# Kernel tuning notes

Measured on AMD Instinct MI355X. Metric: run time of the kernel, lower is better.

Reference implementation:

```python
import jax, jax.numpy as jnp
import numpy as np

R, A, B = 32, 16, 65536  # rules, antecedents, samples


def setup_inputs() -> dict:
    key = jax.random.key(0)
    k1, k2, k3 = jax.random.split(key, 3)
    input_data = jax.random.normal(k1, (B, A), dtype=jnp.float32)
    # abs(normal) like the original init; shift/scale keeps sigmas >= 1 so the
    # product of A Gaussian memberships stays well above fp32 underflow.
    FRB_W = jnp.abs(jax.random.normal(k2, (2 * R * A,), dtype=jnp.float32)) * 0.5 + 1.0
    C = jnp.abs(jax.random.normal(k3, (R, A + 1), dtype=jnp.float32))
    return {"input_data": input_data, "FRB_W": FRB_W, "C": C}


def reference(input_data, FRB_W, C):
    Rn = C.shape[0]
    An = C.shape[1] - 1
    # Faithful to the original indexing: locat_num = A*i + k, Gauss1 mf uses
    # FRB_weights[locat_num : locat_num+2] = (sigma, center) (overlapping windows).
    idx = jnp.arange(Rn)[:, None] * An + jnp.arange(An)[None, :]  # [R, A]
    sigma = FRB_W[idx]          # [R, A]
    center = FRB_W[idx + 1]     # [R, A]
    # Gauss1mf(x, [sigma, c]) = exp(-0.5 * ((x - c) / sigma)^2)
    z = (input_data[:, None, :] - center[None]) / sigma[None]      # [B, R, A]
    u = jnp.exp(-0.5 * z * z)                                      # [B, R, A]
    UU = jnp.prod(u, axis=-1)                                      # [B, R] rule firing strengths
    # TSK first-order consequent: C[:,0] bias + C[:,1:] @ x
    C_help = input_data @ C[:, 1:].T + C[:, 0]                     # [B, R]
    # weighted average over rules
    return jnp.sum(UU * C_help, axis=-1) / jnp.sum(UU, axis=-1)    # [B]
```

## Files before the change

kernel.cpp:

```cpp
#include <hip/hip_runtime.h>

#define RR 32
#define AA 16
#define SPLIT 4
#define RPW (RR / SPLIT)
#define BLOCK 256
#define SPB 64


__global__ __launch_bounds__(512) void tsk_precompute(
    const float* __restrict__ W,
    const float* __restrict__ C,
    float* __restrict__ P)
{
    __shared__ float cpart[RR * AA];
    const float LOG2E = 1.4426950408889634f;
    int t = threadIdx.x;
    if (t < RR * AA) {
        int r = t >> 4, k = t & 15;
        float sig = W[t];
        float c   = W[t + 1];
        float inv2 = 1.0f / (sig * sig);
        P[r * 64 + k]      = -0.5f * inv2 * LOG2E;
        P[r * 64 + 16 + k] = c * inv2 * LOG2E;
        cpart[t]           = -0.5f * c * c * inv2 * LOG2E;
        P[r * 64 + 32 + k] = C[r * (AA + 1) + 1 + k];
    }
    __syncthreads();
    if (t < RR) {
        float s = 0.0f;
        #pragma unroll
        for (int k = 0; k < AA; ++k) s += cpart[t * AA + k];
        P[t * 64 + 49] = s;
        P[t * 64 + 48] = C[t * (AA + 1)];
    }
}

__global__ __launch_bounds__(BLOCK, 4) void tsk_main(
    const float* __restrict__ x,
    const float* __restrict__ P,
    float* __restrict__ out,
    int B)
{
    __shared__ float pnum[SPLIT][SPB];
    __shared__ float pden[SPLIT][SPB];

    const int lane = threadIdx.x & 63;
    const int wv = __builtin_amdgcn_readfirstlane(threadIdx.x >> 6);

    int s = blockIdx.x * SPB + lane;
    int sl = s < B ? s : B - 1;

    const float4* xr = (const float4*)(x + (size_t)sl * AA);
    float4 v0 = xr[0], v1 = xr[1], v2 = xr[2], v3 = xr[3];
    float xv[AA] = { v0.x, v0.y, v0.z, v0.w,
                     v1.x, v1.y, v1.z, v1.w,
                     v2.x, v2.y, v2.z, v2.w,
                     v3.x, v3.y, v3.z, v3.w };
    float x2[AA];
    #pragma unroll
    for (int k = 0; k < AA; ++k) x2[k] = xv[k] * xv[k];

    float num = 0.0f, den = 0.0f;
    const float* pw = P + wv * RPW * 64;
    #pragma unroll 2
    for (int r = 0; r < RPW; ++r) {
        const float* p = pw + r * 64;
        float ea = 0.0f, eb = 0.0f;
        float ch = p[48];
        #pragma unroll
        for (int k = 0; k < AA; ++k) {
            ea = fmaf(p[k],      x2[k], ea);
            eb = fmaf(p[16 + k], xv[k], eb);
            ch = fmaf(p[32 + k], xv[k], ch);
        }
        float w = __builtin_amdgcn_exp2f(ea + eb + p[49]);
        num = fmaf(w, ch, num);
        den += w;
    }

    pnum[wv][lane] = num;
    pden[wv][lane] = den;
    __syncthreads();

    if (threadIdx.x < SPB) {
        int t = threadIdx.x;
        float n = pnum[0][t] + pnum[1][t] + pnum[2][t] + pnum[3][t];
        float d = pden[0][t] + pden[1][t] + pden[2][t] + pden[3][t];
        int so = blockIdx.x * SPB + t;
        if (so < B) out[so] = n * __builtin_amdgcn_rcpf(d);
    }
}

extern "C" void kernel_launch(void* const* d_in, const int* in_sizes, int n_in,
                              void* d_out, int out_size, void* d_ws, size_t ws_size,
                              hipStream_t stream) {
    const float* x = (const float*)d_in[0];
    const float* W = (const float*)d_in[1];
    const float* C = (const float*)d_in[2];
    float* out = (float*)d_out;
    float* P = (float*)d_ws;
    int B = in_sizes[0] / AA;

    tsk_precompute<<<dim3(1), dim3(512), 0, stream>>>(W, C, P);
    tsk_main<<<dim3((B + SPB - 1) / SPB), dim3(BLOCK), 0, stream>>>(x, P, out, B);
}
```

Before: 63.02 us.

## Fuse parameter precompute into main kernel using per-block shared memory

Removes the separate single-block precompute launch. Each block now derives the Gaussian and consequent coefficients itself into LDS and reads them from LDS instead of global memory. This drops one kernel launch and the dependency between the two kernels. In exchange, every block redoes the small precompute and adds two extra barriers and more LDS use per block.

```diff
diff --git a/kernel.cpp b/kernel.cpp
--- a/kernel.cpp
+++ b/kernel.cpp
@@ -7,52 +7,49 @@
 #define BLOCK 256
 #define SPB 64
 
-
-__global__ __launch_bounds__(512) void tsk_precompute(
+__global__ __launch_bounds__(BLOCK, 4) void tsk_fused(
+    const float* __restrict__ x,
     const float* __restrict__ W,
     const float* __restrict__ C,
-    float* __restrict__ P)
-{
-    __shared__ float cpart[RR * AA];
-    const float LOG2E = 1.4426950408889634f;
-    int t = threadIdx.x;
-    if (t < RR * AA) {
-        int r = t >> 4, k = t & 15;
-        float sig = W[t];
-        float c   = W[t + 1];
-        float inv2 = 1.0f / (sig * sig);
-        P[r * 64 + k]      = -0.5f * inv2 * LOG2E;
-        P[r * 64 + 16 + k] = c * inv2 * LOG2E;
-        cpart[t]           = -0.5f * c * c * inv2 * LOG2E;
-        P[r * 64 + 32 + k] = C[r * (AA + 1) + 1 + k];
-    }
-    __syncthreads();
-    if (t < RR) {
-        float s = 0.0f;
-        #pragma unroll
-        for (int k = 0; k < AA; ++k) s += cpart[t * AA + k];
-        P[t * 64 + 49] = s;
-        P[t * 64 + 48] = C[t * (AA + 1)];
-    }
-}
-
-__global__ __launch_bounds__(BLOCK, 4) void tsk_main(
-    const float* __restrict__ x,
-    const float* __restrict__ P,
     float* __restrict__ out,
     int B)
 {
+    __shared__ float Pl[RR * 64];
+    __shared__ float cpart[RR * AA];
     __shared__ float pnum[SPLIT][SPB];
     __shared__ float pden[SPLIT][SPB];
 
-    const int lane = threadIdx.x & 63;
-    const int wv = __builtin_amdgcn_readfirstlane(threadIdx.x >> 6);
+    const float LOG2E = 1.4426950408889634f;
+    const int tid  = threadIdx.x;
+    const int lane = tid & 63;
+    const int wv = __builtin_amdgcn_readfirstlane(tid >> 6);
 
     int s = blockIdx.x * SPB + lane;
     int sl = s < B ? s : B - 1;
-
     const float4* xr = (const float4*)(x + (size_t)sl * AA);
     float4 v0 = xr[0], v1 = xr[1], v2 = xr[2], v3 = xr[3];
+
+    #pragma unroll
+    for (int i = tid; i < RR * AA; i += BLOCK) {
+        int r = i >> 4, k = i & 15;
+        float sig = W[i];
+        float c   = W[i + 1];
+        float inv2 = 1.0f / (sig * sig);
+        Pl[r * 64 + k]      = -0.5f * inv2 * LOG2E;
+        Pl[r * 64 + 16 + k] = c * inv2 * LOG2E;
+        Pl[r * 64 + 32 + k] = C[r * (AA + 1) + 1 + k];
+        cpart[i]            = -0.5f * c * c * inv2 * LOG2E;
+    }
+    __syncthreads();
+    if (tid < RR) {
+        float ssum = 0.0f;
+        #pragma unroll
+        for (int k = 0; k < AA; ++k) ssum += cpart[tid * AA + k];
+        Pl[tid * 64 + 49] = ssum;
+        Pl[tid * 64 + 48] = C[tid * (AA + 1)];
+    }
+    __syncthreads();
+
     float xv[AA] = { v0.x, v0.y, v0.z, v0.w,
                      v1.x, v1.y, v1.z, v1.w,
                      v2.x, v2.y, v2.z, v2.w,
@@ -62,7 +59,7 @@
     for (int k = 0; k < AA; ++k) x2[k] = xv[k] * xv[k];
 
     float num = 0.0f, den = 0.0f;
-    const float* pw = P + wv * RPW * 64;
+    const float* pw = Pl + wv * RPW * 64;
     #pragma unroll 2
     for (int r = 0; r < RPW; ++r) {
         const float* p = pw + r * 64;
@@ -83,11 +80,10 @@
     pden[wv][lane] = den;
     __syncthreads();
 
-    if (threadIdx.x < SPB) {
-        int t = threadIdx.x;
-        float n = pnum[0][t] + pnum[1][t] + pnum[2][t] + pnum[3][t];
-        float d = pden[0][t] + pden[1][t] + pden[2][t] + pden[3][t];
-        int so = blockIdx.x * SPB + t;
+    if (tid < SPB) {
+        float n = pnum[0][tid] + pnum[1][tid] + pnum[2][tid] + pnum[3][tid];
+        float d = pden[0][tid] + pden[1][tid] + pden[2][tid] + pden[3][tid];
+        int so = blockIdx.x * SPB + tid;
         if (so < B) out[so] = n * __builtin_amdgcn_rcpf(d);
     }
 }
@@ -99,9 +95,8 @@
     const float* W = (const float*)d_in[1];
     const float* C = (const float*)d_in[2];
     float* out = (float*)d_out;
-    float* P = (float*)d_ws;
     int B = in_sizes[0] / AA;
+    (void)d_ws; (void)ws_size;
 
-    tsk_precompute<<<dim3(1), dim3(512), 0, stream>>>(W, C, P);
-    tsk_main<<<dim3((B + SPB - 1) / SPB), dim3(BLOCK), 0, stream>>>(x, P, out, B);
+    tsk_fused<<<dim3((B + SPB - 1) / SPB), dim3(BLOCK), 0, stream>>>(x, W, C, out, B);
 }
```

After: 62.73 us. About the same (-0.5%).
